# Kernel tuning notes

Hardware: AMD Instinct MI355X
Metric: run time of the kernel (lower is better)

The kernel has to match this reference:

```python
import jax, jax.numpy as jnp
import numpy as np

S, B, H = 512, 64, 1024


def setup_inputs() -> dict:
    key = jax.random.key(0)
    ks = jax.random.split(key, 9)
    sc = 1.0 / np.sqrt(2 * H)
    return {
        "hidden": jax.random.normal(ks[0], (B, H), jnp.float32),
        "decoder_out": jax.random.normal(ks[1], (B, H), jnp.float32),
        "encoder_states": jax.random.normal(ks[2], (S, B, H), jnp.float32),
        "W_attn": jax.random.uniform(ks[3], (2 * H, 2 * H), jnp.float32, -sc, sc),
        "b_attn": jax.random.uniform(ks[4], (2 * H,), jnp.float32, -sc, sc),
        "W_attn2": jax.random.uniform(ks[5], (1, 2 * H), jnp.float32, -sc, sc),
        "b_attn2": jax.random.uniform(ks[6], (1,), jnp.float32, -sc, sc),
        "W_comb": jax.random.uniform(ks[7], (H, 2 * H), jnp.float32, -sc, sc),
        "b_comb": jax.random.uniform(ks[8], (H,), jnp.float32, -sc, sc),
    }


def reference(hidden, decoder_out, encoder_states, W_attn, b_attn, W_attn2, b_attn2, W_comb, b_comb):
    s, b, h = encoder_states.shape
    # per-timestep cat(hidden, enc_t) -> attn -> tanh -> attn2, fully batched over S
    hid = jnp.broadcast_to(hidden[None], (s, b, h))
    cat = jnp.concatenate([hid, encoder_states], axis=-1)            # [S,B,2H]
    scores = jnp.tanh(cat @ W_attn.T + b_attn) @ W_attn2.T + b_attn2  # [S,B,1]
    scores = scores[..., 0].T                                         # [B,S] (stack dim=1 + squeeze)
    attn_w = jax.nn.softmax(scores, axis=-1)                          # [B,S]
    # bmm([B,1,S], [B,S,H]) -> [B,H]
    applied = jnp.einsum("bs,sbh->bh", attn_w, encoder_states)
    out = jnp.concatenate([decoder_out, applied], axis=-1) @ W_comb.T + b_comb
    out = jnp.tanh(out)
    return out, applied
```

## Files before the change

### kernel.cpp

```cpp
#include <hip/hip_runtime.h>
#include <stdint.h>


typedef __attribute__((ext_vector_type(8))) short bf16x8;
typedef __attribute__((ext_vector_type(4))) float f32x4;

__device__ __forceinline__ float bf2f(uint16_t u) {
  return __uint_as_float(((uint32_t)u) << 16);
}
__device__ __forceinline__ uint16_t f2bf(float x) {
  uint32_t u = __float_as_uint(x);
  u += 0x7fffu + ((u >> 16) & 1u);
  return (uint16_t)(u >> 16);
}
__device__ __forceinline__ uint32_t pk2(float a, float b) {
  return (uint32_t)f2bf(a) | ((uint32_t)f2bf(b) << 16);
}
__device__ __forceinline__ uint4 cvt8(const float* __restrict__ p) {
  const float4 a = *(const float4*)p;
  const float4 b = *(const float4*)(p + 4);
  uint4 r;
  r.x = pk2(a.x, a.y); r.y = pk2(a.z, a.w);
  r.z = pk2(b.x, b.y); r.w = pk2(b.z, b.w);
  return r;
}
__device__ __forceinline__ float tanh_fast(float x) {
  const float e = __expf(2.f * x);
  return __builtin_fmaf(-2.f, __builtin_amdgcn_rcpf(e + 1.f), 1.f);
}
__device__ __forceinline__ void load16(const uint16_t* g, uint16_t* l) {
  __builtin_amdgcn_global_load_lds(
      (const __attribute__((address_space(1))) void*)g,
      (__attribute__((address_space(3))) void*)l, 16, 0, 0);
}

__global__ __launch_bounds__(256)
void init_kernel(float* __restrict__ scores, float* __restrict__ U,
                 const float* __restrict__ ba) {
  const int tid = blockIdx.x * 256 + threadIdx.x;
  scores[tid] = 0.f;
#pragma unroll
  for (int k = 0; k < 4; ++k) {
    const int i = tid * 4 + k;
    U[i] = ba[i & 2047];
  }
}

__global__ __launch_bounds__(256)
void cvt_all_kernel(const float* __restrict__ enc, const float* __restrict__ Wa,
                    const float* __restrict__ Wc,
                    uint16_t* __restrict__ enc_bf, uint16_t* __restrict__ Wa_bf,
                    uint16_t* __restrict__ Wc_bf) {
  const int stride = gridDim.x * 256;
  for (int idx = blockIdx.x * 256 + threadIdx.x; idx < 4718592; idx += stride) {
    if (idx < 4194304) {
      ((uint4*)enc_bf)[idx] = cvt8(enc + (size_t)idx * 8);
    } else if (idx < 4456448) {
      const int k = idx - 4194304;
      const int j = k >> 7, c8 = k & 127;
      ((uint4*)Wa_bf)[k] = cvt8(Wa + (size_t)j * 2048 + 1024 + c8 * 8);
    } else {
      const int k = idx - 4456448;
      ((uint4*)Wc_bf)[k] = cvt8(Wc + (size_t)k * 8);
    }
  }
}

__global__ __launch_bounds__(256)
void gemm_u_kernel(const float* __restrict__ A, const float* __restrict__ B32,
                   float* __restrict__ U) {
  __shared__ __align__(16) uint16_t sA[128 * 32];
  __shared__ __align__(16) uint16_t sB[128 * 32];
  const int t = threadIdx.x, lane = t & 63, wave = t >> 6;
  const int wm = wave >> 1, wn = wave & 1;
  const int bn0 = blockIdx.x * 128;
  const int kbase = blockIdx.y * 256;
  const int srow = t >> 2, scol = (t & 3) * 8;
  const int ar0 = min(srow, 63), ar1 = min(64 + srow, 63);
  f32x4 acc[4][4];
#pragma unroll
  for (int i = 0; i < 4; ++i)
#pragma unroll
    for (int j = 0; j < 4; ++j) acc[i][j] = (f32x4){0.f, 0.f, 0.f, 0.f};
  const int mrow = wm * 64 + (lane & 15);
  const int nrow = wn * 64 + (lane & 15);
  const int kq = (lane >> 4) * 8;
  for (int kk = 0; kk < 8; ++kk) {
    const int k0 = kbase + (kk << 5);
    const uint4 va0 = cvt8(A + (size_t)ar0 * 1024 + scol + k0);
    const uint4 va1 = cvt8(A + (size_t)ar1 * 1024 + scol + k0);
    const uint4 vb0 = cvt8(B32 + (size_t)(bn0 + srow) * 2048 + scol + k0);
    const uint4 vb1 = cvt8(B32 + (size_t)(bn0 + 64 + srow) * 2048 + scol + k0);
    __syncthreads();
    *(uint4*)&sA[t * 8] = va0;
    *(uint4*)&sA[2048 + t * 8] = va1;
    *(uint4*)&sB[t * 8] = vb0;
    *(uint4*)&sB[2048 + t * 8] = vb1;
    __syncthreads();
    bf16x8 af[4], bfr[4];
#pragma unroll
    for (int i = 0; i < 4; ++i) af[i] = *(const bf16x8*)&sA[(mrow + i * 16) * 32 + kq];
#pragma unroll
    for (int j = 0; j < 4; ++j) bfr[j] = *(const bf16x8*)&sB[(nrow + j * 16) * 32 + kq];
#pragma unroll
    for (int i = 0; i < 4; ++i)
#pragma unroll
      for (int j = 0; j < 4; ++j)
        acc[i][j] = __builtin_amdgcn_mfma_f32_16x16x32_bf16(af[i], bfr[j], acc[i][j], 0, 0, 0);
  }
  const int colb = lane & 15, rquad = lane >> 4;
#pragma unroll
  for (int i = 0; i < 4; ++i)
#pragma unroll
    for (int r = 0; r < 4; ++r) {
      const int gm = wm * 64 + i * 16 + rquad * 4 + r;
      if (gm < 64) {
#pragma unroll
        for (int j = 0; j < 4; ++j) {
          const int gn = bn0 + wn * 64 + j * 16 + colb;
          atomicAdd(&U[gm * 2048 + gn], acc[i][j][r]);
        }
      }
    }
}

template <int MODE>
__global__ __launch_bounds__(256)
void gemm_bf_kernel(const uint16_t* __restrict__ A, int lda,
                    const uint16_t* __restrict__ Bm, int ldb,
                    int M, int K,
                    float* __restrict__ outf,
                    const float* __restrict__ Ubias,
                    const float* __restrict__ bias) {
  __shared__ __align__(16) uint16_t sAB[2][128 * 32];
  uint16_t* sA = sAB[0];
  uint16_t* sB = sAB[1];
  float* sU = (float*)sAB;

  const int t = threadIdx.x, lane = t & 63, wave = t >> 6;
  const int wm = wave >> 1, wn = wave & 1;
  const int bm0 = blockIdx.x * 128;
  const int bn0 = blockIdx.y * 128;

  const int srow = t >> 2, scol = (t & 3) * 8;
  const int ar0 = min(bm0 + srow, M - 1);
  const int ar1 = min(bm0 + 64 + srow, M - 1);
  const uint16_t* agp0 = A + (size_t)ar0 * lda + scol;
  const uint16_t* agp1 = A + (size_t)ar1 * lda + scol;
  const uint16_t* bgp0 = Bm + (size_t)(bn0 + srow) * ldb + scol;
  const uint16_t* bgp1 = Bm + (size_t)(bn0 + 64 + srow) * ldb + scol;

  uint16_t* la0 = sA + wave * 512;
  uint16_t* la1 = sA + 2048 + wave * 512;
  uint16_t* lb0 = sB + wave * 512;
  uint16_t* lb1 = sB + 2048 + wave * 512;

  f32x4 acc[4][4];
#pragma unroll
  for (int i = 0; i < 4; ++i)
#pragma unroll
    for (int j = 0; j < 4; ++j) acc[i][j] = (f32x4){0.f, 0.f, 0.f, 0.f};

  const int mrow = wm * 64 + (lane & 15);
  const int nrow = wn * 64 + (lane & 15);
  const int kq = (lane >> 4) * 8;

  const int nsteps = K >> 5;
  for (int kk = 0; kk < nsteps; ++kk) {
    const int k0 = kk << 5;
    load16(agp0 + k0, la0);
    load16(agp1 + k0, la1);
    load16(bgp0 + k0, lb0);
    load16(bgp1 + k0, lb1);
    __syncthreads();

    bf16x8 af[4], bfr[4];
#pragma unroll
    for (int i = 0; i < 4; ++i) af[i] = *(const bf16x8*)&sA[(mrow + i * 16) * 32 + kq];
#pragma unroll
    for (int j = 0; j < 4; ++j) bfr[j] = *(const bf16x8*)&sB[(nrow + j * 16) * 32 + kq];
#pragma unroll
    for (int i = 0; i < 4; ++i)
#pragma unroll
      for (int j = 0; j < 4; ++j)
        acc[i][j] = __builtin_amdgcn_mfma_f32_16x16x32_bf16(af[i], bfr[j], acc[i][j], 0, 0, 0);
    __syncthreads();
  }

  const int colb = lane & 15, rquad = lane >> 4;
  if (MODE == 1) {
#pragma unroll
    for (int q = 0; q < 8; ++q) {
      const int idx = t + q * 256;
      const int b = idx >> 5, c4 = idx & 31;
      ((float4*)sU)[idx] = *(const float4*)&Ubias[b * 2048 + bn0 + c4 * 4];
    }
    __syncthreads();
    float w2f[4];
#pragma unroll
    for (int j = 0; j < 4; ++j) w2f[j] = bias[bn0 + wn * 64 + j * 16 + colb];
#pragma unroll
    for (int i = 0; i < 4; ++i) {
#pragma unroll
      for (int r = 0; r < 4; ++r) {
        const int gm = bm0 + wm * 64 + i * 16 + rquad * 4 + r;
        const int bb = gm & 63;
        float p = 0.f;
#pragma unroll
        for (int j = 0; j < 4; ++j) {
          const float u = sU[bb * 128 + wn * 64 + j * 16 + colb];
          p += tanh_fast(acc[i][j][r] + u) * w2f[j];
        }
        p += __shfl_xor(p, 1);
        p += __shfl_xor(p, 2);
        p += __shfl_xor(p, 4);
        p += __shfl_xor(p, 8);
        if (colb == 0) atomicAdd(outf + gm, p);
      }
    }
  } else {
#pragma unroll
    for (int i = 0; i < 4; ++i)
#pragma unroll
      for (int r = 0; r < 4; ++r) {
        const int gm = bm0 + wm * 64 + i * 16 + rquad * 4 + r;
        if (gm < M) {
#pragma unroll
          for (int j = 0; j < 4; ++j) {
            const int gn = bn0 + wn * 64 + j * 16 + colb;
            outf[gm * 1024 + gn] = tanh_fast(acc[i][j][r] + bias[gn]);
          }
        }
      }
  }
}

__global__ __launch_bounds__(256)
void applied_kernel(const uint16_t* __restrict__ encb, const float* __restrict__ dec,
                    const float* __restrict__ scores,
                    float* __restrict__ out_applied, uint16_t* __restrict__ acat) {
  const int b = blockIdx.x, half = blockIdx.y, t = threadIdx.x;
  const int wave = t >> 6, lane = t & 63;
  __shared__ float w[512];
  __shared__ float red[8];
  float v0 = scores[(size_t)t * 64 + b];
  float v1 = scores[(size_t)(t + 256) * 64 + b];
  float mx = fmaxf(v0, v1);
#pragma unroll
  for (int off = 32; off >= 1; off >>= 1) mx = fmaxf(mx, __shfl_xor(mx, off));
  if (lane == 0) red[wave] = mx;
  __syncthreads();
  mx = fmaxf(fmaxf(red[0], red[1]), fmaxf(red[2], red[3]));
  const float e0 = __expf(v0 - mx), e1 = __expf(v1 - mx);
  float sum = e0 + e1;
#pragma unroll
  for (int off = 32; off >= 1; off >>= 1) sum += __shfl_xor(sum, off);
  if (lane == 0) red[4 + wave] = sum;
  __syncthreads();
  sum = (red[4] + red[5]) + (red[6] + red[7]);
  const float inv = 1.f / sum;
  w[t] = e0 * inv;
  w[t + 256] = e1 * inv;
  __syncthreads();
  const int h = half * 512 + t * 2;
  const uint32_t* base = (const uint32_t*)encb + (size_t)b * 512 + (h >> 1);
  float a0 = 0.f, a1 = 0.f;
#pragma unroll 8
  for (int s = 0; s < 512; ++s) {
    const uint32_t p = base[(size_t)s * 32768];
    a0 += w[s] * bf2f((uint16_t)(p & 0xffffu));
    a1 += w[s] * bf2f((uint16_t)(p >> 16));
  }
  *(float2*)(out_applied + (size_t)b * 1024 + h) = make_float2(a0, a1);
  *(uint32_t*)(acat + (size_t)b * 2048 + 1024 + h) = pk2(a0, a1);
  *(uint32_t*)(acat + (size_t)b * 2048 + h) =
      pk2(dec[(size_t)b * 1024 + h], dec[(size_t)b * 1024 + h + 1]);
}

extern "C" void kernel_launch(void* const* d_in, const int* in_sizes, int n_in,
                              void* d_out, int out_size, void* d_ws, size_t ws_size,
                              hipStream_t stream) {
  const float* hidden  = (const float*)d_in[0];
  const float* dec     = (const float*)d_in[1];
  const float* enc     = (const float*)d_in[2];
  const float* W_attn  = (const float*)d_in[3];
  const float* b_attn  = (const float*)d_in[4];
  const float* W_attn2 = (const float*)d_in[5];
  const float* W_comb  = (const float*)d_in[7];
  const float* b_comb  = (const float*)d_in[8];
  float* outp = (float*)d_out;

  char* ws = (char*)d_ws;
  float*    scores = (float*)(ws + 0);
  float*    U      = (float*)(ws + 131072);
  uint16_t* acat   = (uint16_t*)(ws + 655360);
  uint16_t* enc_bf = (uint16_t*)(ws + 1048576);
  uint16_t* Wa_bf  = (uint16_t*)(ws + 68157440);
  uint16_t* Wc_bf  = (uint16_t*)(ws + 72351744);

  init_kernel<<<128, 256, 0, stream>>>(scores, U, b_attn);
  cvt_all_kernel<<<4608, 256, 0, stream>>>(enc, W_attn, W_comb, enc_bf, Wa_bf, Wc_bf);
  gemm_u_kernel<<<dim3(16, 4), 256, 0, stream>>>(hidden, W_attn, U);
  gemm_bf_kernel<1><<<dim3(256, 16), 256, 0, stream>>>(
      enc_bf, 1024, Wa_bf, 1024, 32768, 1024, scores, U, W_attn2);
  applied_kernel<<<dim3(64, 2), 256, 0, stream>>>(enc_bf, dec, scores, outp + 65536, acat);
  gemm_bf_kernel<2><<<dim3(1, 8), 256, 0, stream>>>(
      acat, 2048, Wc_bf, 2048, 64, 2048, outp, nullptr, b_comb);
}
```

Baseline: 525.3 us.

## Double-buffer GEMM LDS, split applied reduction over S, split-K final GEMM

```diff
diff --git a/kernel.cpp b/kernel.cpp
--- a/kernel.cpp
+++ b/kernel.cpp
@@ -132,28 +132,24 @@
                     float* __restrict__ outf,
                     const float* __restrict__ Ubias,
                     const float* __restrict__ bias) {
-  __shared__ __align__(16) uint16_t sAB[2][128 * 32];
-  uint16_t* sA = sAB[0];
-  uint16_t* sB = sAB[1];
+  __shared__ __align__(16) uint16_t sAB[2][2][4096];
   float* sU = (float*)sAB;
 
   const int t = threadIdx.x, lane = t & 63, wave = t >> 6;
   const int wm = wave >> 1, wn = wave & 1;
   const int bm0 = blockIdx.x * 128;
   const int bn0 = blockIdx.y * 128;
+  const int kbase = (MODE == 3) ? (int)blockIdx.z * 512 : 0;
+  const int nsteps = ((MODE == 3) ? 512 : K) >> 5;
 
   const int srow = t >> 2, scol = (t & 3) * 8;
   const int ar0 = min(bm0 + srow, M - 1);
   const int ar1 = min(bm0 + 64 + srow, M - 1);
-  const uint16_t* agp0 = A + (size_t)ar0 * lda + scol;
-  const uint16_t* agp1 = A + (size_t)ar1 * lda + scol;
-  const uint16_t* bgp0 = Bm + (size_t)(bn0 + srow) * ldb + scol;
-  const uint16_t* bgp1 = Bm + (size_t)(bn0 + 64 + srow) * ldb + scol;
-
-  uint16_t* la0 = sA + wave * 512;
-  uint16_t* la1 = sA + 2048 + wave * 512;
-  uint16_t* lb0 = sB + wave * 512;
-  uint16_t* lb1 = sB + 2048 + wave * 512;
+  const uint16_t* agp0 = A + (size_t)ar0 * lda + scol + kbase;
+  const uint16_t* agp1 = A + (size_t)ar1 * lda + scol + kbase;
+  const uint16_t* bgp0 = Bm + (size_t)(bn0 + srow) * ldb + scol + kbase;
+  const uint16_t* bgp1 = Bm + (size_t)(bn0 + 64 + srow) * ldb + scol + kbase;
+  const int so = wave * 512;
 
   f32x4 acc[4][4];
 #pragma unroll
@@ -165,15 +161,38 @@
   const int nrow = wn * 64 + (lane & 15);
   const int kq = (lane >> 4) * 8;
 
-  const int nsteps = K >> 5;
-  for (int kk = 0; kk < nsteps; ++kk) {
-    const int k0 = kk << 5;
-    load16(agp0 + k0, la0);
-    load16(agp1 + k0, la1);
-    load16(bgp0 + k0, lb0);
-    load16(bgp1 + k0, lb1);
-    __syncthreads();
-
+  load16(agp0, &sAB[0][0][so]);
+  load16(agp1, &sAB[0][0][2048 + so]);
+  load16(bgp0, &sAB[0][1][so]);
+  load16(bgp1, &sAB[0][1][2048 + so]);
+  __syncthreads();
+
+  int cur = 0;
+  for (int kk = 0; kk < nsteps - 1; ++kk) {
+    const int k0 = (kk + 1) << 5;
+    load16(agp0 + k0, &sAB[cur ^ 1][0][so]);
+    load16(agp1 + k0, &sAB[cur ^ 1][0][2048 + so]);
+    load16(bgp0 + k0, &sAB[cur ^ 1][1][so]);
+    load16(bgp1 + k0, &sAB[cur ^ 1][1][2048 + so]);
+
+    const uint16_t* sA = sAB[cur][0];
+    const uint16_t* sB = sAB[cur][1];
+    bf16x8 af[4], bfr[4];
+#pragma unroll
+    for (int i = 0; i < 4; ++i) af[i] = *(const bf16x8*)&sA[(mrow + i * 16) * 32 + kq];
+#pragma unroll
+    for (int j = 0; j < 4; ++j) bfr[j] = *(const bf16x8*)&sB[(nrow + j * 16) * 32 + kq];
+#pragma unroll
+    for (int i = 0; i < 4; ++i)
+#pragma unroll
+      for (int j = 0; j < 4; ++j)
+        acc[i][j] = __builtin_amdgcn_mfma_f32_16x16x32_bf16(af[i], bfr[j], acc[i][j], 0, 0, 0);
+    __syncthreads();
+    cur ^= 1;
+  }
+  {
+    const uint16_t* sA = sAB[cur][0];
+    const uint16_t* sB = sAB[cur][1];
     bf16x8 af[4], bfr[4];
 #pragma unroll
     for (int i = 0; i < 4; ++i) af[i] = *(const bf16x8*)&sA[(mrow + i * 16) * 32 + kq];
@@ -218,7 +237,7 @@
         if (colb == 0) atomicAdd(outf + gm, p);
       }
     }
-  } else {
+  } else if (MODE == 2) {
 #pragma unroll
     for (int i = 0; i < 4; ++i)
 #pragma unroll
@@ -232,17 +251,34 @@
           }
         }
       }
+  } else {
+    const float bsc = (blockIdx.z == 0) ? 1.f : 0.f;
+#pragma unroll
+    for (int i = 0; i < 4; ++i)
+#pragma unroll
+      for (int r = 0; r < 4; ++r) {
+        const int gm = bm0 + wm * 64 + i * 16 + rquad * 4 + r;
+        if (gm < M) {
+#pragma unroll
+          for (int j = 0; j < 4; ++j) {
+            const int gn = bn0 + wn * 64 + j * 16 + colb;
+            atomicAdd(outf + gm * 1024 + gn, acc[i][j][r] + bsc * bias[gn]);
+          }
+        }
+      }
   }
 }
 
 __global__ __launch_bounds__(256)
 void applied_kernel(const uint16_t* __restrict__ encb, const float* __restrict__ dec,
                     const float* __restrict__ scores,
-                    float* __restrict__ out_applied, uint16_t* __restrict__ acat) {
-  const int b = blockIdx.x, half = blockIdx.y, t = threadIdx.x;
+                    float* __restrict__ out_applied, uint16_t* __restrict__ acat,
+                    float* __restrict__ out_acc) {
+  const int b = blockIdx.x, chunk = blockIdx.y, t = threadIdx.x;
   const int wave = t >> 6, lane = t & 63;
   __shared__ float w[512];
   __shared__ float red[8];
+  __shared__ float2 part2[256];
   float v0 = scores[(size_t)t * 64 + b];
   float v1 = scores[(size_t)(t + 256) * 64 + b];
   float mx = fmaxf(v0, v1);
@@ -262,19 +298,40 @@
   w[t] = e0 * inv;
   w[t + 256] = e1 * inv;
   __syncthreads();
-  const int h = half * 512 + t * 2;
+  const int hp = t & 31, sq = t >> 5;
+  const int h = chunk * 64 + hp * 2;
   const uint32_t* base = (const uint32_t*)encb + (size_t)b * 512 + (h >> 1);
   float a0 = 0.f, a1 = 0.f;
 #pragma unroll 8
-  for (int s = 0; s < 512; ++s) {
+  for (int s = sq * 64; s < sq * 64 + 64; ++s) {
     const uint32_t p = base[(size_t)s * 32768];
     a0 += w[s] * bf2f((uint16_t)(p & 0xffffu));
     a1 += w[s] * bf2f((uint16_t)(p >> 16));
   }
-  *(float2*)(out_applied + (size_t)b * 1024 + h) = make_float2(a0, a1);
-  *(uint32_t*)(acat + (size_t)b * 2048 + 1024 + h) = pk2(a0, a1);
-  *(uint32_t*)(acat + (size_t)b * 2048 + h) =
-      pk2(dec[(size_t)b * 1024 + h], dec[(size_t)b * 1024 + h + 1]);
+  part2[t] = make_float2(a0, a1);
+  __syncthreads();
+  if (t < 32) {
+    a0 = 0.f; a1 = 0.f;
+#pragma unroll
+    for (int k = 0; k < 8; ++k) {
+      const float2 pp = part2[t + 32 * k];
+      a0 += pp.x; a1 += pp.y;
+    }
+    *(float2*)(out_applied + (size_t)b * 1024 + h) = make_float2(a0, a1);
+    *(uint32_t*)(acat + (size_t)b * 2048 + 1024 + h) = pk2(a0, a1);
+    *(uint32_t*)(acat + (size_t)b * 2048 + h) =
+        pk2(dec[(size_t)b * 1024 + h], dec[(size_t)b * 1024 + h + 1]);
+    *(float2*)(out_acc + (size_t)b * 1024 + h) = make_float2(0.f, 0.f);
+  }
+}
+
+__global__ __launch_bounds__(256)
+void tanh_kernel(const float* __restrict__ acc, float* __restrict__ outp) {
+  const int i = blockIdx.x * 256 + threadIdx.x;
+  float4 v = ((const float4*)acc)[i];
+  v.x = tanh_fast(v.x); v.y = tanh_fast(v.y);
+  v.z = tanh_fast(v.z); v.w = tanh_fast(v.w);
+  ((float4*)outp)[i] = v;
 }
 
 extern "C" void kernel_launch(void* const* d_in, const int* in_sizes, int n_in,
@@ -293,6 +350,7 @@
   char* ws = (char*)d_ws;
   float*    scores = (float*)(ws + 0);
   float*    U      = (float*)(ws + 131072);
+  float*    out_acc= (float*)(ws + 131072);
   uint16_t* acat   = (uint16_t*)(ws + 655360);
   uint16_t* enc_bf = (uint16_t*)(ws + 1048576);
   uint16_t* Wa_bf  = (uint16_t*)(ws + 68157440);
@@ -303,7 +361,9 @@
   gemm_u_kernel<<<dim3(16, 4), 256, 0, stream>>>(hidden, W_attn, U);
   gemm_bf_kernel<1><<<dim3(256, 16), 256, 0, stream>>>(
       enc_bf, 1024, Wa_bf, 1024, 32768, 1024, scores, U, W_attn2);
-  applied_kernel<<<dim3(64, 2), 256, 0, stream>>>(enc_bf, dec, scores, outp + 65536, acat);
-  gemm_bf_kernel<2><<<dim3(1, 8), 256, 0, stream>>>(
-      acat, 2048, Wc_bf, 2048, 64, 2048, outp, nullptr, b_comb);
-}
+  applied_kernel<<<dim3(64, 16), 256, 0, stream>>>(enc_bf, dec, scores,
+                                                   outp + 65536, acat, out_acc);
+  gemm_bf_kernel<3><<<dim3(1, 8, 4), 256, 0, stream>>>(
+      acat, 2048, Wc_bf, 2048, 64, 2048, out_acc, nullptr, b_comb);
+  tanh_kernel<<<64, 256, 0, stream>>>(out_acc, outp);
+}
```

New measurement: 475.4 us. 9.5% less time.
